# Performance work log

Measured on AMD Instinct MI355X. Metric: run time of the kernel, lower is better.

Reference implementation:

```python
import jax, jax.numpy as jnp
import numpy as np
from jax import lax

B, L, NCH, NQ, NL, FW, NCLS = 256, 3000, 4, 8, 2, 128, 5
BN_EPS = 1e-5


def setup_inputs() -> dict:
    key = jax.random.key(0)
    ks = jax.random.split(key, 24)
    rn = lambda k, shape, s=0.05: jax.random.normal(k, shape, jnp.float32) * s
    inp = {}
    inp['x'] = jax.random.normal(ks[0], (B, NCH, L), jnp.float32)
    inp['conv1_w'] = rn(ks[1], (32, NCH, 7)); inp['conv1_b'] = rn(ks[2], (32,))
    inp['bn1_g'] = 1.0 + rn(ks[3], (32,)); inp['bn1_b'] = rn(ks[3], (32,))
    inp['conv2_w'] = rn(ks[4], (64, 32, 7)); inp['conv2_b'] = rn(ks[5], (64,))
    inp['bn2_g'] = 1.0 + rn(ks[6], (64,)); inp['bn2_b'] = rn(ks[6], (64,))
    inp['conv3_w'] = rn(ks[7], (128, 64, 7)); inp['conv3_b'] = rn(ks[8], (128,))
    inp['bn3_g'] = 1.0 + rn(ks[9], (128,)); inp['bn3_b'] = rn(ks[9], (128,))
    inp['conv4_w'] = rn(ks[10], (128, 128, 7)); inp['conv4_b'] = rn(ks[11], (128,))
    inp['bn4_g'] = 1.0 + rn(ks[12], (128,)); inp['bn4_b'] = rn(ks[12], (128,))
    inp['fc_w'] = rn(ks[13], (FW, 128)); inp['fc_b'] = rn(ks[14], (FW,))
    inp['ang_w'] = rn(ks[15], (NQ, FW)); inp['ang_b'] = rn(ks[16], (NQ,))
    # TorchLayer default init: uniform in [0, 2*pi)
    inp['qw'] = jax.random.uniform(ks[17], (NL, NQ, 3), jnp.float32, 0.0, 2.0 * np.pi)
    inp['h1_w'] = rn(ks[18], (64, NQ)); inp['h1_b'] = rn(ks[19], (64,))
    inp['h2_w'] = rn(ks[20], (NCLS, 64)); inp['h2_b'] = rn(ks[21], (NCLS,))
    return inp


def _conv1d(x, w, b):
    y = lax.conv_general_dilated(x, w, (1,), [(3, 3)], dimension_numbers=('NCH', 'OIH', 'NCH'))
    return y + b[None, :, None]


def _bn(x, g, b):  # eval-mode BN: running_mean=0, running_var=1
    inv = 1.0 / np.sqrt(1.0 + BN_EPS)
    return x * (g * inv)[None, :, None] + b[None, :, None]


def _maxpool4(x):
    return lax.reduce_window(x, -jnp.inf, lax.max, (1, 1, 4), (1, 1, 4), 'VALID')


def _apply_1q(state, U, w, batched):
    # state: (B, 2**NQ); wire 0 = most significant bit (PennyLane convention)
    bs = state.shape[0]
    st = state.reshape(bs, 2 ** w, 2, -1)
    if batched:
        new = jnp.einsum('sab,slbr->slar', U, st)
    else:
        new = jnp.einsum('ab,slbr->slar', U, st)
    return new.reshape(bs, -1)


def _apply_cnot(state, c, t):
    bs = state.shape[0]
    q1, q2 = min(c, t), max(c, t)
    s = state.reshape(bs, 2 ** q1, 2, 2 ** (q2 - q1 - 1), 2, -1)
    ci, ti = (2, 4) if c < t else (4, 2)
    c0 = lax.index_in_dim(s, 0, ci, keepdims=True)
    c1 = jnp.flip(lax.index_in_dim(s, 1, ci, keepdims=True), axis=ti)
    return jnp.concatenate([c0, c1], axis=ci).reshape(bs, -1)


def _rot_matrix(phi, th, om):
    # PennyLane Rot(phi, theta, omega) = RZ(omega) RY(theta) RZ(phi)
    cm, sm = jnp.cos(th / 2), jnp.sin(th / 2)
    m00 = jnp.exp(-0.5j * (phi + om)) * cm
    m01 = -jnp.exp(0.5j * (phi - om)) * sm
    m10 = jnp.exp(-0.5j * (phi - om)) * sm
    m11 = jnp.exp(0.5j * (phi + om)) * cm
    return jnp.stack([jnp.stack([m00, m01]), jnp.stack([m10, m11])]).astype(jnp.complex64)


def _qsim(angles, qw):
    bs = angles.shape[0]
    dim = 2 ** NQ
    state = jnp.zeros((bs, dim), jnp.complex64).at[:, 0].set(1.0)
    # AngleEmbedding: RY(angle_w) on each wire (batched matrices)
    c, s = jnp.cos(angles / 2), jnp.sin(angles / 2)
    for w in range(NQ):
        U = jnp.stack([jnp.stack([c[:, w], -s[:, w]], -1),
                       jnp.stack([s[:, w], c[:, w]], -1)], -2).astype(jnp.complex64)
        state = _apply_1q(state, U, w, batched=True)
    # StronglyEntanglingLayers: Rot on each wire, then CNOT ring with range r
    for l in range(NL):
        for w in range(NQ):
            U = _rot_matrix(qw[l, w, 0], qw[l, w, 1], qw[l, w, 2])
            state = _apply_1q(state, U, w, batched=False)
        r = (l % (NQ - 1)) + 1
        for i in range(NQ):
            state = _apply_cnot(state, i, (i + r) % NQ)
    probs = state.real ** 2 + state.imag ** 2
    z = [probs.reshape(bs, 2 ** w, 2, -1)[:, :, 0].sum((1, 2))
         - probs.reshape(bs, 2 ** w, 2, -1)[:, :, 1].sum((1, 2)) for w in range(NQ)]
    return jnp.stack(z, -1)  # (B, NQ)


def reference(x, conv1_w, conv1_b, bn1_g, bn1_b, conv2_w, conv2_b, bn2_g, bn2_b,
              conv3_w, conv3_b, bn3_g, bn3_b, conv4_w, conv4_b, bn4_g, bn4_b,
              fc_w, fc_b, ang_w, ang_b, qw, h1_w, h1_b, h2_w, h2_b):
    h = jax.nn.relu(_bn(_conv1d(x, conv1_w, conv1_b), bn1_g, bn1_b))
    h = jax.nn.relu(_bn(_conv1d(h, conv2_w, conv2_b), bn2_g, bn2_b))
    h = _maxpool4(h)
    h = jax.nn.relu(_bn(_conv1d(h, conv3_w, conv3_b), bn3_g, bn3_b))
    h = _maxpool4(h)
    h = jax.nn.relu(_bn(_conv1d(h, conv4_w, conv4_b), bn4_g, bn4_b))
    h = h.mean(-1)  # AdaptiveAvgPool1d(1) + Flatten -> (B, 128)
    h = jax.nn.relu(h @ fc_w.T + fc_b)  # Dropout is identity in eval
    raw = h @ ang_w.T + ang_b
    angles = np.pi * jnp.tanh(raw)
    q = _qsim(angles, qw)
    h2 = jax.nn.relu(q @ h1_w.T + h1_b)
    return h2 @ h2_w.T + h2_b
```

## Files before the change

### kernel.cpp

```cpp
#include <hip/hip_runtime.h>
#include <hip/hip_bf16.h>

#define BN_INV 0.9999950000375f
#define PI_F   3.14159265358979f

typedef __attribute__((ext_vector_type(8))) short s16x8;
typedef __attribute__((ext_vector_type(4))) float f32x4;
typedef __attribute__((ext_vector_type(4))) unsigned short u16x4;

__device__ inline unsigned short f2bf(float f) {
  union { float f; unsigned u; } v; v.f = f;
  unsigned r = v.u + 0x7fffu + ((v.u >> 16) & 1u);
  return (unsigned short)(r >> 16);
}

__global__ __launch_bounds__(256) void k_pack(
    const float* __restrict__ w1, const float* __restrict__ w2,
    const float* __restrict__ w3, const float* __restrict__ w4,
    unsigned short* __restrict__ w1p, unsigned short* __restrict__ w2p,
    unsigned short* __restrict__ w3p, unsigned short* __restrict__ w4p,
    float* __restrict__ h4)
{
  int e = blockIdx.x * 256 + threadIdx.x;
  if (e < 2048) {
    int co = e >> 6, k = e & 63, kk = k >> 3, ci = k & 7;
    w1p[e] = (ci < 4 && kk < 7) ? f2bf(w1[co * 28 + ci * 7 + kk]) : (unsigned short)0;
  } else if (e < 16384) {
    int t = e - 2048; int co = t / 224, k = t % 224, kk = k >> 5, ci = k & 31;
    w2p[t] = f2bf(w2[co * 224 + ci * 7 + kk]);
  } else if (e < 73728) {
    int t = e - 16384; int co = t / 448, k = t % 448, kk = k >> 6, ci = k & 63;
    w3p[t] = f2bf(w3[co * 448 + ci * 7 + kk]);
  } else if (e < 188416) {
    int t = e - 73728; int co = t / 896, k = t % 896, kk = k >> 7, ci = k & 127;
    w4p[t] = f2bf(w4[co * 896 + ci * 7 + kk]);
  } else if (e < 221184) {
    h4[e - 188416] = 0.f;
  }
}

__global__ __launch_bounds__(256) void k_conv1(
    const float* __restrict__ x, const unsigned short* __restrict__ w1p,
    const float* __restrict__ cb, const float* __restrict__ bng,
    const float* __restrict__ bnb, unsigned short* __restrict__ h1t)
{
  __shared__ __align__(16) char lds[520 * 16 + 4096 + 256];
  float* scs = (float*)(lds + 520 * 16 + 4096);
  const int tid = threadIdx.x;
  const int b = blockIdx.y;
  const int l0 = blockIdx.x * 512;

  for (int r = tid; r < 519; r += 256) {
    int gr = l0 + r - 3;
    s16x8 v;
    if (gr >= 0 && gr < 3000) {
      const float* xr = x + b * 4 * 3000 + gr;
      v[0] = (short)f2bf(xr[0]);
      v[1] = (short)f2bf(xr[3000]);
      v[2] = (short)f2bf(xr[6000]);
      v[3] = (short)f2bf(xr[9000]);
      v[4] = 0; v[5] = 0; v[6] = 0; v[7] = 0;
    } else {
      for (int i = 0; i < 8; ++i) v[i] = 0;
    }
    *(s16x8*)(lds + r * 16) = v;
  }
  {
    int co = tid >> 3, c = tid & 7;
    s16x8 v = *(const s16x8*)(w1p + co * 64 + c * 8);
    *(s16x8*)(lds + 8320 + ((co * 128 + c * 16) ^ ((co & 7) << 4))) = v;
  }
  if (tid < 32) {
    float sc = bng[tid] * BN_INV;
    scs[tid * 2] = sc;
    scs[tid * 2 + 1] = fmaf(cb[tid], sc, bnb[tid]);
  }
  __syncthreads();

  const int w = tid >> 6, l = tid & 63, lr = l & 15, g = l >> 4;
  const int wp = w * 128;
  f32x4 acc[2][8];
  for (int m = 0; m < 2; ++m)
    for (int n = 0; n < 8; ++n)
      for (int i = 0; i < 4; ++i) acc[m][n][i] = 0.f;

  #pragma unroll
  for (int s = 0; s < 2; ++s) {
    s16x8 a[2], bf[8];
    #pragma unroll
    for (int m = 0; m < 2; ++m) {
      int co = m * 16 + lr;
      a[m] = *(const s16x8*)(lds + 8320 + ((co * 128 + s * 64 + g * 16) ^ ((co & 7) << 4)));
    }
    #pragma unroll
    for (int n = 0; n < 8; ++n) {
      int row = wp + n * 16 + lr + s * 4 + g;
      bf[n] = *(const s16x8*)(lds + row * 16);
    }
    #pragma unroll
    for (int m = 0; m < 2; ++m)
      #pragma unroll
      for (int n = 0; n < 8; ++n)
        acc[m][n] = __builtin_amdgcn_mfma_f32_16x16x32_bf16(a[m], bf[n], acc[m][n], 0, 0, 0);
  }

  #pragma unroll
  for (int m = 0; m < 2; ++m) {
    int co0 = m * 16 + g * 4;
    float sc[4], sh[4];
    #pragma unroll
    for (int j = 0; j < 4; ++j) { sc[j] = scs[(co0 + j) * 2]; sh[j] = scs[(co0 + j) * 2 + 1]; }
    #pragma unroll
    for (int n = 0; n < 8; ++n) {
      int gp = l0 + wp + n * 16 + lr;
      if (gp < 3000) {
        u16x4 o;
        #pragma unroll
        for (int j = 0; j < 4; ++j)
          o[j] = f2bf(fmaxf(fmaf(acc[m][n][j], sc[j], sh[j]), 0.f));
        *(u16x4*)(h1t + (b * 3000 + gp) * 32 + co0) = o;
      }
    }
  }
}

__global__ __launch_bounds__(256) void k_conv2(
    const unsigned short* __restrict__ h1t, const unsigned short* __restrict__ w2p,
    const float* __restrict__ cb, const float* __restrict__ bng,
    const float* __restrict__ bnb, unsigned short* __restrict__ h2pt)
{
  __shared__ __align__(16) char lds[46080];
  float* scs = (float*)(lds + 45568);
  const int tid = threadIdx.x, b = blockIdx.y, bg = blockIdx.x;

  for (int e = tid; e < 1792; e += 256) {
    int co = e / 28, c = e % 28;
    s16x8 v = *(const s16x8*)(w2p + co * 224 + c * 8);
    *(s16x8*)(lds + 16896 + ((co * 448 + c * 16) ^ ((co & 7) << 4))) = v;
  }
  if (tid < 64) {
    float sc = bng[tid] * BN_INV;
    scs[tid * 2] = sc;
    scs[tid * 2 + 1] = fmaf(cb[tid], sc, bnb[tid]);
  }
  {
    int l0 = bg * 1024;
    #pragma unroll
    for (int i = 0; i < 5; ++i) {
      int e = tid + i * 256;
      if (e < 1048) {
        int r = e >> 2, c = e & 3, gr = l0 - 3 + r;
        s16x8 v;
        if (gr >= 0 && gr < 3000) v = *(const s16x8*)(h1t + (b * 3000 + gr) * 32 + c * 8);
        else for (int q = 0; q < 8; ++q) v[q] = 0;
        *(s16x8*)(lds + ((r * 64 + c * 16) ^ ((r & 7) << 4))) = v;
      }
    }
  }
  __syncthreads();

  const int w = tid >> 6, l = tid & 63, lr = l & 15, g = l >> 4;
  const int wp = w * 64;

  for (int t = 0; t < 4; ++t) {
    const int l0 = bg * 1024 + t * 256;

    s16x8 xr[5];
    if (t < 3) {
      int nl0 = l0 + 256;
      #pragma unroll
      for (int i = 0; i < 5; ++i) {
        for (int q = 0; q < 8; ++q) xr[i][q] = 0;
        int e = tid + i * 256;
        if (e < 1048) {
          int r = e >> 2, c = e & 3, gr = nl0 - 3 + r;
          if (gr >= 0 && gr < 3000)
            xr[i] = *(const s16x8*)(h1t + (b * 3000 + gr) * 32 + c * 8);
        }
      }
    }

    f32x4 acc[4][4];
    for (int m = 0; m < 4; ++m)
      for (int n = 0; n < 4; ++n)
        for (int i = 0; i < 4; ++i) acc[m][n][i] = 0.f;

    #pragma unroll
    for (int s = 0; s < 7; ++s) {
      s16x8 a[4], bf[4];
      #pragma unroll
      for (int m = 0; m < 4; ++m) {
        int co = m * 16 + lr;
        a[m] = *(const s16x8*)(lds + 16896 + ((co * 448 + s * 64 + g * 16) ^ ((co & 7) << 4)));
      }
      #pragma unroll
      for (int n = 0; n < 4; ++n) {
        int row = wp + n * 16 + lr + s;
        bf[n] = *(const s16x8*)(lds + ((row * 64 + g * 16) ^ ((row & 7) << 4)));
      }
      #pragma unroll
      for (int m = 0; m < 4; ++m)
        #pragma unroll
        for (int n = 0; n < 4; ++n)
          acc[m][n] = __builtin_amdgcn_mfma_f32_16x16x32_bf16(a[m], bf[n], acc[m][n], 0, 0, 0);
    }

    #pragma unroll
    for (int m = 0; m < 4; ++m) {
      int co0 = m * 16 + g * 4;
      float sc[4], sh[4];
      #pragma unroll
      for (int j = 0; j < 4; ++j) { sc[j] = scs[(co0 + j) * 2]; sh[j] = scs[(co0 + j) * 2 + 1]; }
      #pragma unroll
      for (int n = 0; n < 4; ++n) {
        u16x4 o;
        #pragma unroll
        for (int j = 0; j < 4; ++j) {
          float tv = fmaxf(fmaf(acc[m][n][j], sc[j], sh[j]), 0.f);
          float t1 = fmaxf(tv, __shfl_xor(tv, 1));
          float t2 = fmaxf(t1, __shfl_xor(t1, 2));
          o[j] = f2bf(t2);
        }
        int pp = (l0 + wp + n * 16 + lr) >> 2;
        if ((l & 3) == 0 && pp < 750)
          *(u16x4*)(h2pt + (b * 750 + pp) * 64 + co0) = o;
      }
    }

    __syncthreads();
    if (t < 3) {
      #pragma unroll
      for (int i = 0; i < 5; ++i) {
        int e = tid + i * 256;
        if (e < 1048) {
          int r = e >> 2, c = e & 3;
          *(s16x8*)(lds + ((r * 64 + c * 16) ^ ((r & 7) << 4))) = xr[i];
        }
      }
    }
    __syncthreads();
  }
}

__global__ __launch_bounds__(256) void k_conv3(
    const unsigned short* __restrict__ h2pt, const unsigned short* __restrict__ w3p,
    const float* __restrict__ cb, const float* __restrict__ bng,
    const float* __restrict__ bnb, unsigned short* __restrict__ h3pt)
{
  __shared__ __align__(16) char lds[75776];
  float* scs = (float*)(lds + 74752);
  const int tid = threadIdx.x, b = blockIdx.y, ch = blockIdx.x;
  const int cg0 = ch * 64;

  for (int e = tid; e < 3584; e += 256) {
    int co = e / 56, c = e % 56;
    s16x8 v = *(const s16x8*)(w3p + (cg0 + co) * 448 + c * 8);
    *(s16x8*)(lds + 17408 + ((co * 896 + c * 16) ^ ((co & 7) << 4))) = v;
  }
  if (tid < 64) {
    int co = cg0 + tid;
    float sc = bng[co] * BN_INV;
    scs[tid * 2] = sc;
    scs[tid * 2 + 1] = fmaf(cb[co], sc, bnb[co]);
  }
  {
    #pragma unroll
    for (int i = 0; i < 5; ++i) {
      int e = tid + i * 256;
      if (e < 1072) {
        int r = e >> 3, c = e & 7, gr = r - 3;
        s16x8 v;
        if (gr >= 0 && gr < 750) v = *(const s16x8*)(h2pt + (b * 750 + gr) * 64 + c * 8);
        else for (int q = 0; q < 8; ++q) v[q] = 0;
        *(s16x8*)(lds + ((r * 128 + c * 16) ^ ((r & 7) << 4))) = v;
      }
    }
  }
  __syncthreads();

  const int w = tid >> 6, l = tid & 63, lr = l & 15, g = l >> 4;
  const int wp = w * 32;

  for (int t = 0; t < 6; ++t) {
    const int l0 = t * 128;

    s16x8 xr[5];
    if (t < 5) {
      int nl0 = l0 + 128;
      #pragma unroll
      for (int i = 0; i < 5; ++i) {
        for (int q = 0; q < 8; ++q) xr[i][q] = 0;
        int e = tid + i * 256;
        if (e < 1072) {
          int r = e >> 3, c = e & 7, gr = nl0 - 3 + r;
          if (gr >= 0 && gr < 750)
            xr[i] = *(const s16x8*)(h2pt + (b * 750 + gr) * 64 + c * 8);
        }
      }
    }

    f32x4 acc[4][2];
    for (int m = 0; m < 4; ++m)
      for (int n = 0; n < 2; ++n)
        for (int i = 0; i < 4; ++i) acc[m][n][i] = 0.f;

    #pragma unroll
    for (int sl = 0; sl < 14; ++sl) {
      int kk = sl >> 1, cib = (sl & 1) * 32;
      s16x8 a[4], bf[2];
      #pragma unroll
      for (int m = 0; m < 4; ++m) {
        int co = m * 16 + lr;
        a[m] = *(const s16x8*)(lds + 17408 + ((co * 896 + sl * 64 + g * 16) ^ ((co & 7) << 4)));
      }
      #pragma unroll
      for (int n = 0; n < 2; ++n) {
        int row = wp + n * 16 + lr + kk;
        bf[n] = *(const s16x8*)(lds + ((row * 128 + cib * 2 + g * 16) ^ ((row & 7) << 4)));
      }
      #pragma unroll
      for (int m = 0; m < 4; ++m)
        #pragma unroll
        for (int n = 0; n < 2; ++n)
          acc[m][n] = __builtin_amdgcn_mfma_f32_16x16x32_bf16(a[m], bf[n], acc[m][n], 0, 0, 0);
    }

    #pragma unroll
    for (int m = 0; m < 4; ++m) {
      int co0 = m * 16 + g * 4;
      float sc[4], sh[4];
      #pragma unroll
      for (int j = 0; j < 4; ++j) { sc[j] = scs[(co0 + j) * 2]; sh[j] = scs[(co0 + j) * 2 + 1]; }
      #pragma unroll
      for (int n = 0; n < 2; ++n) {
        u16x4 o;
        #pragma unroll
        for (int j = 0; j < 4; ++j) {
          float tv = fmaxf(fmaf(acc[m][n][j], sc[j], sh[j]), 0.f);
          float t1 = fmaxf(tv, __shfl_xor(tv, 1));
          float t2 = fmaxf(t1, __shfl_xor(t1, 2));
          o[j] = f2bf(t2);
        }
        int pp = (l0 + wp + n * 16 + lr) >> 2;
        if ((l & 3) == 0 && pp < 187)
          *(u16x4*)(h3pt + (b * 187 + pp) * 128 + cg0 + co0) = o;
      }
    }

    __syncthreads();
    if (t < 5) {
      #pragma unroll
      for (int i = 0; i < 5; ++i) {
        int e = tid + i * 256;
        if (e < 1072) {
          int r = e >> 3, c = e & 7;
          *(s16x8*)(lds + ((r * 128 + c * 16) ^ ((r & 7) << 4))) = xr[i];
        }
      }
    }
    __syncthreads();
  }
}

__global__ __launch_bounds__(256) void k_conv4(
    const unsigned short* __restrict__ h3pt, const unsigned short* __restrict__ w4p,
    const float* __restrict__ cb, const float* __restrict__ bng,
    const float* __restrict__ bnb, float* __restrict__ h4)
{
  __shared__ __align__(16) char lds[79872];
  float* scs = (float*)(lds + 79360);
  const int tid = threadIdx.x, b = blockIdx.y, ch = blockIdx.x;
  const int cg0 = ch * 64;

  #pragma unroll
  for (int i = 0; i < 13; ++i) {
    int e = tid + i * 256;
    if (e < 3168) {
      int r = e >> 4, c = e & 15, gr = r - 3;
      s16x8 v;
      if (gr >= 0 && gr < 187) v = *(const s16x8*)(h3pt + (b * 187 + gr) * 128 + c * 8);
      else for (int q = 0; q < 8; ++q) v[q] = 0;
      *(s16x8*)(lds + ((r * 256 + c * 16) ^ ((r & 7) << 4))) = v;
    }
  }
  for (int e = tid; e < 1792; e += 256) {
    int co = e / 28, c = e % 28;
    s16x8 v = *(const s16x8*)(w4p + (cg0 + co) * 896 + c * 8);
    *(s16x8*)(lds + 50688 + ((co * 448 + c * 16) ^ ((co & 7) << 4))) = v;
  }
  if (tid < 64) {
    int co = cg0 + tid;
    float sc = bng[co] * BN_INV;
    scs[tid * 2] = sc;
    scs[tid * 2 + 1] = fmaf(cb[co], sc, bnb[co]);
  }
  __syncthreads();

  const int w = tid >> 6, l = tid & 63, lr = l & 15, g = l >> 4;
  const int co_off = (w & 1) * 32, pos_off = (w >> 1) * 96;

  f32x4 acc[2][6];
  for (int m = 0; m < 2; ++m)
    for (int n = 0; n < 6; ++n)
      for (int i = 0; i < 4; ++i) acc[m][n][i] = 0.f;

  for (int chunk = 0; chunk < 4; ++chunk) {
    s16x8 wr[7];
    if (chunk < 3) {
      #pragma unroll
      for (int i = 0; i < 7; ++i) {
        int e = tid + i * 256;
        int co = e / 28, c = e % 28;
        wr[i] = *(const s16x8*)(w4p + (cg0 + co) * 896 + (chunk + 1) * 224 + c * 8);
      }
    }
    #pragma unroll
    for (int sl = 0; sl < 7; ++sl) {
      int k0 = chunk * 224 + sl * 32;
      int kk = k0 >> 7, cib = k0 & 127;
      s16x8 a[2], bf[6];
      #pragma unroll
      for (int m = 0; m < 2; ++m) {
        int co = co_off + m * 16 + lr;
        a[m] = *(const s16x8*)(lds + 50688 + ((co * 448 + sl * 64 + g * 16) ^ ((co & 7) << 4)));
      }
      #pragma unroll
      for (int n = 0; n < 6; ++n) {
        int row = pos_off + n * 16 + lr + kk;
        bf[n] = *(const s16x8*)(lds + ((row * 256 + cib * 2 + g * 16) ^ ((row & 7) << 4)));
      }
      #pragma unroll
      for (int m = 0; m < 2; ++m)
        #pragma unroll
        for (int n = 0; n < 6; ++n)
          acc[m][n] = __builtin_amdgcn_mfma_f32_16x16x32_bf16(a[m], bf[n], acc[m][n], 0, 0, 0);
    }
    __syncthreads();
    if (chunk < 3) {
      #pragma unroll
      for (int i = 0; i < 7; ++i) {
        int e = tid + i * 256;
        int co = e / 28, c = e % 28;
        *(s16x8*)(lds + 50688 + ((co * 448 + c * 16) ^ ((co & 7) << 4))) = wr[i];
      }
    }
    __syncthreads();
  }

  float psum[2][4];
  for (int m = 0; m < 2; ++m)
    for (int j = 0; j < 4; ++j) psum[m][j] = 0.f;
  #pragma unroll
  for (int m = 0; m < 2; ++m) {
    int col = co_off + m * 16 + g * 4;
    #pragma unroll
    for (int n = 0; n < 6; ++n) {
      int pos_g = pos_off + n * 16 + lr;
      #pragma unroll
      for (int j = 0; j < 4; ++j) {
        float tv = fmaxf(fmaf(acc[m][n][j], scs[(col + j) * 2], scs[(col + j) * 2 + 1]), 0.f);
        if (pos_g < 187) psum[m][j] += tv;
      }
    }
  }
  #pragma unroll
  for (int m = 0; m < 2; ++m)
    #pragma unroll
    for (int j = 0; j < 4; ++j) {
      float v = psum[m][j];
      v += __shfl_xor(v, 1);
      v += __shfl_xor(v, 2);
      v += __shfl_xor(v, 4);
      v += __shfl_xor(v, 8);
      if (lr == 0)
        atomicAdd(&h4[b * 128 + cg0 + co_off + m * 16 + g * 4 + j], v);
    }
}

__global__ __launch_bounds__(64) void k_head(
    const float* __restrict__ h4, const float* __restrict__ fc_w,
    const float* __restrict__ fc_b, const float* __restrict__ ang_w,
    const float* __restrict__ ang_b, const float* __restrict__ qw,
    const float* __restrict__ h1_w, const float* __restrict__ h1_b,
    const float* __restrict__ h2_w, const float* __restrict__ h2_b,
    float* __restrict__ out)
{
  const int lane = threadIdx.x;
  const int b = blockIdx.x;

  float hv0 = h4[b * 128 + lane] * (1.0f / 187.0f);
  float hv1 = h4[b * 128 + 64 + lane] * (1.0f / 187.0f);

  float a0 = fc_b[lane], a1 = fc_b[lane + 64];
  {
    const float* w0 = fc_w + lane * 128;
    const float* w1 = fc_w + (lane + 64) * 128;
    #pragma unroll
    for (int k = 0; k < 64; ++k) {
      float hk = __shfl(hv0, k);
      a0 = fmaf(hk, w0[k], a0);
      a1 = fmaf(hk, w1[k], a1);
    }
    #pragma unroll
    for (int k = 0; k < 64; ++k) {
      float hk = __shfl(hv1, k);
      a0 = fmaf(hk, w0[64 + k], a0);
      a1 = fmaf(hk, w1[64 + k], a1);
    }
  }
  float f0 = fmaxf(a0, 0.f), f1 = fmaxf(a1, 0.f);

  float rcw[8], rsw[8];
  #pragma unroll
  for (int o = 0; o < 8; ++o) {
    float p = fmaf(f0, ang_w[o * 128 + lane], f1 * ang_w[o * 128 + 64 + lane]);
    #pragma unroll
    for (int m = 1; m < 64; m <<= 1) p += __shfl_xor(p, m);
    float aa = PI_F * tanhf(ang_b[o] + p);
    rcw[o] = cosf(0.5f * aa);
    rsw[o] = sinf(0.5f * aa);
  }

  float r0, r1, r2, r3, r4, r5, r6, r7;
  {
    int gq = lane & 15;
    float phi = qw[gq * 3], th = qw[gq * 3 + 1], om = qw[gq * 3 + 2];
    float cm = cosf(0.5f * th), sm = sinf(0.5f * th);
    float ap = 0.5f * (phi + om), bm = 0.5f * (phi - om);
    float ca = cosf(ap), sa = sinf(ap), cb2 = cosf(bm), sb2 = sinf(bm);
    r0 = cm * ca;   r1 = -cm * sa;
    r2 = -sm * cb2; r3 = -sm * sb2;
    r4 = sm * cb2;  r5 = -sm * sb2;
    r6 = cm * ca;   r7 = cm * sa;
  }

  float2 st[4];
  st[0] = make_float2((lane == 0) ? 1.f : 0.f, 0.f);
  st[1] = make_float2(0.f, 0.f);
  st[2] = make_float2(0.f, 0.f);
  st[3] = make_float2(0.f, 0.f);

  auto ry_lane = [&](int lx, float c, float s) {
    #pragma unroll
    for (int j = 0; j < 4; ++j) {
      float ox = __shfl_xor(st[j].x, lx);
      float oy = __shfl_xor(st[j].y, lx);
      bool hi = (lane & lx) != 0;
      float a0x = hi ? ox : st[j].x, a0y = hi ? oy : st[j].y;
      float a1x = hi ? st[j].x : ox, a1y = hi ? st[j].y : oy;
      float cA = hi ? s : c, cB = hi ? c : -s;
      st[j].x = cA * a0x + cB * a1x;
      st[j].y = cA * a0y + cB * a1y;
    }
  };
#define RY_SLOT(J0, J1, c, s) { \
    float2 A = st[J0], B = st[J1]; \
    st[J0].x = (c) * A.x - (s) * B.x; st[J0].y = (c) * A.y - (s) * B.y; \
    st[J1].x = (s) * A.x + (c) * B.x; st[J1].y = (s) * A.y + (c) * B.y; }

  ry_lane(32, rcw[0], rsw[0]);
  ry_lane(16, rcw[1], rsw[1]);
  ry_lane(8,  rcw[2], rsw[2]);
  ry_lane(4,  rcw[3], rsw[3]);
  ry_lane(2,  rcw[4], rsw[4]);
  ry_lane(1,  rcw[5], rsw[5]);
  RY_SLOT(0, 2, rcw[6], rsw[6]); RY_SLOT(1, 3, rcw[6], rsw[6]);
  RY_SLOT(0, 1, rcw[7], rsw[7]); RY_SLOT(2, 3, rcw[7], rsw[7]);

  auto rot_lane = [&](int gi, int lx) {
    float m00x = __shfl(r0, gi), m00y = __shfl(r1, gi);
    float m01x = __shfl(r2, gi), m01y = __shfl(r3, gi);
    float m10x = __shfl(r4, gi), m10y = __shfl(r5, gi);
    float m11x = __shfl(r6, gi), m11y = __shfl(r7, gi);
    #pragma unroll
    for (int j = 0; j < 4; ++j) {
      float ox = __shfl_xor(st[j].x, lx);
      float oy = __shfl_xor(st[j].y, lx);
      bool hi = (lane & lx) != 0;
      float a0x = hi ? ox : st[j].x, a0y = hi ? oy : st[j].y;
      float a1x = hi ? st[j].x : ox, a1y = hi ? st[j].y : oy;
      float cx = hi ? m10x : m00x, cy = hi ? m10y : m00y;
      float dx = hi ? m11x : m01x, dy = hi ? m11y : m01y;
      st[j].x = cx * a0x - cy * a0y + dx * a1x - dy * a1y;
      st[j].y = cx * a0y + cy * a0x + dx * a1y + dy * a1x;
    }
  };
#define ROT_SLOT(J0, J1) { \
    float2 A = st[J0], B = st[J1]; \
    st[J0].x = m00x * A.x - m00y * A.y + m01x * B.x - m01y * B.y; \
    st[J0].y = m00x * A.y + m00y * A.x + m01x * B.y + m01y * B.x; \
    st[J1].x = m10x * A.x - m10y * A.y + m11x * B.x - m11y * B.y; \
    st[J1].y = m10x * A.y + m10y * A.x + m11x * B.y + m11y * B.x; }
  auto rot_slot = [&](int gi, int bit) {
    float m00x = __shfl(r0, gi), m00y = __shfl(r1, gi);
    float m01x = __shfl(r2, gi), m01y = __shfl(r3, gi);
    float m10x = __shfl(r4, gi), m10y = __shfl(r5, gi);
    float m11x = __shfl(r6, gi), m11y = __shfl(r7, gi);
    if (bit == 1) { ROT_SLOT(0, 2) ROT_SLOT(1, 3) }
    else          { ROT_SLOT(0, 1) ROT_SLOT(2, 3) }
  };

  auto cnot = [&](int cmask, int tmask) {
    bool cb0, cb1, cb2, cb3;
    if (cmask >= 4) {
      bool cbl = (lane & (cmask >> 2)) != 0;
      cb0 = cbl; cb1 = cbl; cb2 = cbl; cb3 = cbl;
    } else {
      cb0 = false;
      cb1 = (1 & cmask) != 0;
      cb2 = (2 & cmask) != 0;
      cb3 = (3 & cmask) != 0;
    }
    if (tmask >= 4) {
      int lx = tmask >> 2;
      { float ox = __shfl_xor(st[0].x, lx), oy = __shfl_xor(st[0].y, lx); if (cb0) { st[0].x = ox; st[0].y = oy; } }
      { float ox = __shfl_xor(st[1].x, lx), oy = __shfl_xor(st[1].y, lx); if (cb1) { st[1].x = ox; st[1].y = oy; } }
      { float ox = __shfl_xor(st[2].x, lx), oy = __shfl_xor(st[2].y, lx); if (cb2) { st[2].x = ox; st[2].y = oy; } }
      { float ox = __shfl_xor(st[3].x, lx), oy = __shfl_xor(st[3].y, lx); if (cb3) { st[3].x = ox; st[3].y = oy; } }
    } else {
      float2 o0 = st[0], o1 = st[1], o2 = st[2], o3 = st[3];
      if (tmask == 2) {
        if (cb0) st[0] = o2;
        if (cb1) st[1] = o3;
        if (cb2) st[2] = o0;
        if (cb3) st[3] = o1;
      } else {
        if (cb0) st[0] = o1;
        if (cb1) st[1] = o0;
        if (cb2) st[2] = o3;
        if (cb3) st[3] = o2;
      }
    }
  };

  #pragma unroll
  for (int lay = 0; lay < 2; ++lay) {
    rot_lane(lay * 8 + 0, 32);
    rot_lane(lay * 8 + 1, 16);
    rot_lane(lay * 8 + 2, 8);
    rot_lane(lay * 8 + 3, 4);
    rot_lane(lay * 8 + 4, 2);
    rot_lane(lay * 8 + 5, 1);
    rot_slot(lay * 8 + 6, 1);
    rot_slot(lay * 8 + 7, 0);
    int r = lay + 1;
    #pragma unroll
    for (int i = 0; i < 8; ++i) {
      int c = i, t = (i + r) & 7;
      cnot(1 << (7 - c), 1 << (7 - t));
    }
  }

  float p0 = st[0].x * st[0].x + st[0].y * st[0].y;
  float p1 = st[1].x * st[1].x + st[1].y * st[1].y;
  float p2 = st[2].x * st[2].x + st[2].y * st[2].y;
  float p3 = st[3].x * st[3].x + st[3].y * st[3].y;
  float sAll = p0 + p1 + p2 + p3;
  float zp[8];
  zp[0] = (lane & 32) ? -sAll : sAll;
  zp[1] = (lane & 16) ? -sAll : sAll;
  zp[2] = (lane & 8)  ? -sAll : sAll;
  zp[3] = (lane & 4)  ? -sAll : sAll;
  zp[4] = (lane & 2)  ? -sAll : sAll;
  zp[5] = (lane & 1)  ? -sAll : sAll;
  zp[6] = (p0 + p1) - (p2 + p3);
  zp[7] = (p0 - p1) + (p2 - p3);
  #pragma unroll
  for (int o = 0; o < 8; ++o) {
    #pragma unroll
    for (int m = 1; m < 64; m <<= 1) zp[o] += __shfl_xor(zp[o], m);
  }

  float ah = h1_b[lane];
  const float* hw = h1_w + lane * 8;
  #pragma unroll
  for (int k = 0; k < 8; ++k) ah = fmaf(zp[k], hw[k], ah);
  float hh = fmaxf(ah, 0.f);

  #pragma unroll
  for (int o = 0; o < 5; ++o) {
    float v = hh * h2_w[o * 64 + lane];
    #pragma unroll
    for (int m = 1; m < 64; m <<= 1) v += __shfl_xor(v, m);
    if (lane == 0) out[b * 5 + o] = v + h2_b[o];
  }
#undef RY_SLOT
#undef ROT_SLOT
}

extern "C" void kernel_launch(void* const* d_in, const int* in_sizes, int n_in,
                              void* d_out, int out_size, void* d_ws, size_t ws_size,
                              hipStream_t stream) {
  (void)in_sizes; (void)n_in; (void)out_size; (void)ws_size;
  const float* x    = (const float*)d_in[0];
  const float* c1w  = (const float*)d_in[1];
  const float* c1b  = (const float*)d_in[2];
  const float* b1g  = (const float*)d_in[3];
  const float* b1b  = (const float*)d_in[4];
  const float* c2w  = (const float*)d_in[5];
  const float* c2b  = (const float*)d_in[6];
  const float* b2g  = (const float*)d_in[7];
  const float* b2b  = (const float*)d_in[8];
  const float* c3w  = (const float*)d_in[9];
  const float* c3b  = (const float*)d_in[10];
  const float* b3g  = (const float*)d_in[11];
  const float* b3b  = (const float*)d_in[12];
  const float* c4w  = (const float*)d_in[13];
  const float* c4b  = (const float*)d_in[14];
  const float* b4g  = (const float*)d_in[15];
  const float* b4b  = (const float*)d_in[16];
  const float* fcw  = (const float*)d_in[17];
  const float* fcb  = (const float*)d_in[18];
  const float* angw = (const float*)d_in[19];
  const float* angb = (const float*)d_in[20];
  const float* qw   = (const float*)d_in[21];
  const float* h1w  = (const float*)d_in[22];
  const float* h1b  = (const float*)d_in[23];
  const float* h2w  = (const float*)d_in[24];
  const float* h2b  = (const float*)d_in[25];

  char* wsb = (char*)d_ws;
  unsigned short* w1p  = (unsigned short*)(wsb + 0);
  unsigned short* w2p  = (unsigned short*)(wsb + 4096);
  unsigned short* w3p  = (unsigned short*)(wsb + 32768);
  unsigned short* w4p  = (unsigned short*)(wsb + 147456);
  float*          h4   = (float*)(wsb + 393216);
  unsigned short* h1t  = (unsigned short*)(wsb + 1048576);
  unsigned short* h2pt = (unsigned short*)(wsb + 52428800);
  unsigned short* h3pt = (unsigned short*)(wsb + 79691776);

  k_pack<<<dim3(864), 256, 0, stream>>>(c1w, c2w, c3w, c4w, w1p, w2p, w3p, w4p, h4);
  k_conv1<<<dim3(6, 256), 256, 0, stream>>>(x, w1p, c1b, b1g, b1b, h1t);
  k_conv2<<<dim3(3, 256), 256, 0, stream>>>(h1t, w2p, c2b, b2g, b2b, h2pt);
  k_conv3<<<dim3(2, 256), 256, 0, stream>>>(h2pt, w3p, c3b, b3g, b3b, h3pt);
  k_conv4<<<dim3(2, 256), 256, 0, stream>>>(h3pt, w4p, c4b, b4g, b4b, h4);
  k_head<<<dim3(256), 64, 0, stream>>>(h4, fcw, fcb, angw, angb, qw,
                                       h1w, h1b, h2w, h2b, (float*)d_out);
}
```

Measured before the change: 251.9 us.

## Swap MFMA operand roles and split conv2/conv3 into one tile per block

Conv2 and conv3 now give each block a single position tile instead of looping over several tiles with register-prefetch double buffering. The grids grow from 3 and 2 blocks per batch to 12. The MFMA operands are swapped so positions map to the accumulator's row dimension. That makes the 4-wide maxpool a purely in-register max over the accumulator lanes, with no cross-lane shuffles, and conv4's mean reduction uses fewer shuffles and atomics. The cost is that weights are reloaded into LDS for every tile and stores become scalar 16-bit writes rather than 4-wide vectors.

```diff
diff --git a/kernel.cpp b/kernel.cpp
--- a/kernel.cpp
+++ b/kernel.cpp
@@ -131,8 +131,17 @@
 {
   __shared__ __align__(16) char lds[46080];
   float* scs = (float*)(lds + 45568);
-  const int tid = threadIdx.x, b = blockIdx.y, bg = blockIdx.x;
-
+  const int tid = threadIdx.x, b = blockIdx.y;
+  const int l0 = blockIdx.x * 256;
+
+  for (int e = tid; e < 1048; e += 256) {
+    int r = e >> 2, c = e & 3;
+    int gr = l0 + r - 3;
+    s16x8 v;
+    if (gr >= 0 && gr < 3000) v = *(const s16x8*)(h1t + (b * 3000 + gr) * 32 + c * 8);
+    else for (int i = 0; i < 8; ++i) v[i] = 0;
+    *(s16x8*)(lds + ((r * 64 + c * 16) ^ ((r & 7) << 4))) = v;
+  }
   for (int e = tid; e < 1792; e += 256) {
     int co = e / 28, c = e % 28;
     s16x8 v = *(const s16x8*)(w2p + co * 224 + c * 8);
@@ -143,102 +152,53 @@
     scs[tid * 2] = sc;
     scs[tid * 2 + 1] = fmaf(cb[tid], sc, bnb[tid]);
   }
-  {
-    int l0 = bg * 1024;
-    #pragma unroll
-    for (int i = 0; i < 5; ++i) {
-      int e = tid + i * 256;
-      if (e < 1048) {
-        int r = e >> 2, c = e & 3, gr = l0 - 3 + r;
-        s16x8 v;
-        if (gr >= 0 && gr < 3000) v = *(const s16x8*)(h1t + (b * 3000 + gr) * 32 + c * 8);
-        else for (int q = 0; q < 8; ++q) v[q] = 0;
-        *(s16x8*)(lds + ((r * 64 + c * 16) ^ ((r & 7) << 4))) = v;
-      }
-    }
-  }
   __syncthreads();
 
   const int w = tid >> 6, l = tid & 63, lr = l & 15, g = l >> 4;
   const int wp = w * 64;
-
-  for (int t = 0; t < 4; ++t) {
-    const int l0 = bg * 1024 + t * 256;
-
-    s16x8 xr[5];
-    if (t < 3) {
-      int nl0 = l0 + 256;
-      #pragma unroll
-      for (int i = 0; i < 5; ++i) {
-        for (int q = 0; q < 8; ++q) xr[i][q] = 0;
-        int e = tid + i * 256;
-        if (e < 1048) {
-          int r = e >> 2, c = e & 3, gr = nl0 - 3 + r;
-          if (gr >= 0 && gr < 3000)
-            xr[i] = *(const s16x8*)(h1t + (b * 3000 + gr) * 32 + c * 8);
-        }
-      }
-    }
-
-    f32x4 acc[4][4];
+  f32x4 acc[4][4];
+  for (int m = 0; m < 4; ++m)
+    for (int n = 0; n < 4; ++n)
+      for (int i = 0; i < 4; ++i) acc[m][n][i] = 0.f;
+
+  #pragma unroll
+  for (int s = 0; s < 7; ++s) {
+    s16x8 xa[4], wb[4];
+    #pragma unroll
+    for (int m = 0; m < 4; ++m) {
+      int row = wp + m * 16 + lr + s;
+      xa[m] = *(const s16x8*)(lds + ((row * 64 + g * 16) ^ ((row & 7) << 4)));
+    }
+    #pragma unroll
+    for (int n = 0; n < 4; ++n) {
+      int co = n * 16 + lr;
+      wb[n] = *(const s16x8*)(lds + 16896 + ((co * 448 + s * 64 + g * 16) ^ ((co & 7) << 4)));
+    }
+    #pragma unroll
     for (int m = 0; m < 4; ++m)
+      #pragma unroll
       for (int n = 0; n < 4; ++n)
-        for (int i = 0; i < 4; ++i) acc[m][n][i] = 0.f;
-
-    #pragma unroll
-    for (int s = 0; s < 7; ++s) {
-      s16x8 a[4], bf[4];
-      #pragma unroll
-      for (int m = 0; m < 4; ++m) {
-        int co = m * 16 + lr;
-        a[m] = *(const s16x8*)(lds + 16896 + ((co * 448 + s * 64 + g * 16) ^ ((co & 7) << 4)));
-      }
+        acc[m][n] = __builtin_amdgcn_mfma_f32_16x16x32_bf16(xa[m], wb[n], acc[m][n], 0, 0, 0);
+  }
+
+  float sc[4], sh[4];
+  #pragma unroll
+  for (int n = 0; n < 4; ++n) {
+    sc[n] = scs[(n * 16 + lr) * 2];
+    sh[n] = scs[(n * 16 + lr) * 2 + 1];
+  }
+  #pragma unroll
+  for (int m = 0; m < 4; ++m) {
+    int pp = (l0 + wp + m * 16 + g * 4) >> 2;
+    if (pp < 750) {
+      unsigned short* orow = h2pt + (b * 750 + pp) * 64 + lr;
       #pragma unroll
       for (int n = 0; n < 4; ++n) {
-        int row = wp + n * 16 + lr + s;
-        bf[n] = *(const s16x8*)(lds + ((row * 64 + g * 16) ^ ((row & 7) << 4)));
-      }
-      #pragma unroll
-      for (int m = 0; m < 4; ++m)
-        #pragma unroll
-        for (int n = 0; n < 4; ++n)
-          acc[m][n] = __builtin_amdgcn_mfma_f32_16x16x32_bf16(a[m], bf[n], acc[m][n], 0, 0, 0);
-    }
-
-    #pragma unroll
-    for (int m = 0; m < 4; ++m) {
-      int co0 = m * 16 + g * 4;
-      float sc[4], sh[4];
-      #pragma unroll
-      for (int j = 0; j < 4; ++j) { sc[j] = scs[(co0 + j) * 2]; sh[j] = scs[(co0 + j) * 2 + 1]; }
-      #pragma unroll
-      for (int n = 0; n < 4; ++n) {
-        u16x4 o;
-        #pragma unroll
-        for (int j = 0; j < 4; ++j) {
-          float tv = fmaxf(fmaf(acc[m][n][j], sc[j], sh[j]), 0.f);
-          float t1 = fmaxf(tv, __shfl_xor(tv, 1));
-          float t2 = fmaxf(t1, __shfl_xor(t1, 2));
-          o[j] = f2bf(t2);
-        }
-        int pp = (l0 + wp + n * 16 + lr) >> 2;
-        if ((l & 3) == 0 && pp < 750)
-          *(u16x4*)(h2pt + (b * 750 + pp) * 64 + co0) = o;
-      }
-    }
-
-    __syncthreads();
-    if (t < 3) {
-      #pragma unroll
-      for (int i = 0; i < 5; ++i) {
-        int e = tid + i * 256;
-        if (e < 1048) {
-          int r = e >> 2, c = e & 3;
-          *(s16x8*)(lds + ((r * 64 + c * 16) ^ ((r & 7) << 4))) = xr[i];
-        }
-      }
-    }
-    __syncthreads();
+        float v = fmaxf(fmaxf(acc[m][n][0], acc[m][n][1]),
+                        fmaxf(acc[m][n][2], acc[m][n][3]));
+        orow[n * 16] = f2bf(fmaxf(fmaf(v, sc[n], sh[n]), 0.f));
+      }
+    }
   }
 }
 
@@ -249,9 +209,18 @@
 {
   __shared__ __align__(16) char lds[75776];
   float* scs = (float*)(lds + 74752);
-  const int tid = threadIdx.x, b = blockIdx.y, ch = blockIdx.x;
-  const int cg0 = ch * 64;
-
+  const int tid = threadIdx.x, b = blockIdx.y;
+  const int tile = blockIdx.x >> 1, ch = blockIdx.x & 1;
+  const int l0 = tile * 128, cg0 = ch * 64;
+
+  for (int e = tid; e < 1072; e += 256) {
+    int r = e >> 3, c = e & 7;
+    int gr = l0 + r - 3;
+    s16x8 v;
+    if (gr >= 0 && gr < 750) v = *(const s16x8*)(h2pt + (b * 750 + gr) * 64 + c * 8);
+    else for (int i = 0; i < 8; ++i) v[i] = 0;
+    *(s16x8*)(lds + ((r * 128 + c * 16) ^ ((r & 7) << 4))) = v;
+  }
   for (int e = tid; e < 3584; e += 256) {
     int co = e / 56, c = e % 56;
     s16x8 v = *(const s16x8*)(w3p + (cg0 + co) * 448 + c * 8);
@@ -263,102 +232,54 @@
     scs[tid * 2] = sc;
     scs[tid * 2 + 1] = fmaf(cb[co], sc, bnb[co]);
   }
-  {
-    #pragma unroll
-    for (int i = 0; i < 5; ++i) {
-      int e = tid + i * 256;
-      if (e < 1072) {
-        int r = e >> 3, c = e & 7, gr = r - 3;
-        s16x8 v;
-        if (gr >= 0 && gr < 750) v = *(const s16x8*)(h2pt + (b * 750 + gr) * 64 + c * 8);
-        else for (int q = 0; q < 8; ++q) v[q] = 0;
-        *(s16x8*)(lds + ((r * 128 + c * 16) ^ ((r & 7) << 4))) = v;
-      }
-    }
-  }
   __syncthreads();
 
   const int w = tid >> 6, l = tid & 63, lr = l & 15, g = l >> 4;
   const int wp = w * 32;
-
-  for (int t = 0; t < 6; ++t) {
-    const int l0 = t * 128;
-
-    s16x8 xr[5];
-    if (t < 5) {
-      int nl0 = l0 + 128;
-      #pragma unroll
-      for (int i = 0; i < 5; ++i) {
-        for (int q = 0; q < 8; ++q) xr[i][q] = 0;
-        int e = tid + i * 256;
-        if (e < 1072) {
-          int r = e >> 3, c = e & 7, gr = nl0 - 3 + r;
-          if (gr >= 0 && gr < 750)
-            xr[i] = *(const s16x8*)(h2pt + (b * 750 + gr) * 64 + c * 8);
-        }
-      }
-    }
-
-    f32x4 acc[4][2];
-    for (int m = 0; m < 4; ++m)
-      for (int n = 0; n < 2; ++n)
-        for (int i = 0; i < 4; ++i) acc[m][n][i] = 0.f;
-
-    #pragma unroll
-    for (int sl = 0; sl < 14; ++sl) {
-      int kk = sl >> 1, cib = (sl & 1) * 32;
-      s16x8 a[4], bf[2];
-      #pragma unroll
-      for (int m = 0; m < 4; ++m) {
-        int co = m * 16 + lr;
-        a[m] = *(const s16x8*)(lds + 17408 + ((co * 896 + sl * 64 + g * 16) ^ ((co & 7) << 4)));
-      }
-      #pragma unroll
-      for (int n = 0; n < 2; ++n) {
-        int row = wp + n * 16 + lr + kk;
-        bf[n] = *(const s16x8*)(lds + ((row * 128 + cib * 2 + g * 16) ^ ((row & 7) << 4)));
-      }
-      #pragma unroll
-      for (int m = 0; m < 4; ++m)
-        #pragma unroll
-        for (int n = 0; n < 2; ++n)
-          acc[m][n] = __builtin_amdgcn_mfma_f32_16x16x32_bf16(a[m], bf[n], acc[m][n], 0, 0, 0);
-    }
-
-    #pragma unroll
-    for (int m = 0; m < 4; ++m) {
-      int co0 = m * 16 + g * 4;
-      float sc[4], sh[4];
-      #pragma unroll
-      for (int j = 0; j < 4; ++j) { sc[j] = scs[(co0 + j) * 2]; sh[j] = scs[(co0 + j) * 2 + 1]; }
-      #pragma unroll
-      for (int n = 0; n < 2; ++n) {
-        u16x4 o;
-        #pragma unroll
-        for (int j = 0; j < 4; ++j) {
-          float tv = fmaxf(fmaf(acc[m][n][j], sc[j], sh[j]), 0.f);
-          float t1 = fmaxf(tv, __shfl_xor(tv, 1));
-          float t2 = fmaxf(t1, __shfl_xor(t1, 2));
-          o[j] = f2bf(t2);
-        }
-        int pp = (l0 + wp + n * 16 + lr) >> 2;
-        if ((l & 3) == 0 && pp < 187)
-          *(u16x4*)(h3pt + (b * 187 + pp) * 128 + cg0 + co0) = o;
-      }
-    }
-
-    __syncthreads();
-    if (t < 5) {
-      #pragma unroll
-      for (int i = 0; i < 5; ++i) {
-        int e = tid + i * 256;
-        if (e < 1072) {
-          int r = e >> 3, c = e & 7;
-          *(s16x8*)(lds + ((r * 128 + c * 16) ^ ((r & 7) << 4))) = xr[i];
-        }
-      }
-    }
-    __syncthreads();
+  f32x4 acc[2][4];
+  for (int m = 0; m < 2; ++m)
+    for (int n = 0; n < 4; ++n)
+      for (int i = 0; i < 4; ++i) acc[m][n][i] = 0.f;
+
+  #pragma unroll
+  for (int sl = 0; sl < 14; ++sl) {
+    int kk = sl >> 1, cib = (sl & 1) * 32;
+    s16x8 xa[2], wb[4];
+    #pragma unroll
+    for (int m = 0; m < 2; ++m) {
+      int row = wp + m * 16 + lr + kk;
+      xa[m] = *(const s16x8*)(lds + ((row * 128 + cib * 2 + g * 16) ^ ((row & 7) << 4)));
+    }
+    #pragma unroll
+    for (int n = 0; n < 4; ++n) {
+      int co = n * 16 + lr;
+      wb[n] = *(const s16x8*)(lds + 17408 + ((co * 896 + sl * 64 + g * 16) ^ ((co & 7) << 4)));
+    }
+    #pragma unroll
+    for (int m = 0; m < 2; ++m)
+      #pragma unroll
+      for (int n = 0; n < 4; ++n)
+        acc[m][n] = __builtin_amdgcn_mfma_f32_16x16x32_bf16(xa[m], wb[n], acc[m][n], 0, 0, 0);
+  }
+
+  float sc[4], sh[4];
+  #pragma unroll
+  for (int n = 0; n < 4; ++n) {
+    sc[n] = scs[(n * 16 + lr) * 2];
+    sh[n] = scs[(n * 16 + lr) * 2 + 1];
+  }
+  #pragma unroll
+  for (int m = 0; m < 2; ++m) {
+    int pp = (l0 + wp + m * 16 + g * 4) >> 2;
+    if (pp < 187) {
+      unsigned short* orow = h3pt + (b * 187 + pp) * 128 + cg0 + lr;
+      #pragma unroll
+      for (int n = 0; n < 4; ++n) {
+        float v = fmaxf(fmaxf(acc[m][n][0], acc[m][n][1]),
+                        fmaxf(acc[m][n][2], acc[m][n][3]));
+        orow[n * 16] = f2bf(fmaxf(fmaf(v, sc[n], sh[n]), 0.f));
+      }
+    }
   }
 }
 
@@ -397,11 +318,11 @@
   __syncthreads();
 
   const int w = tid >> 6, l = tid & 63, lr = l & 15, g = l >> 4;
-  const int co_off = (w & 1) * 32, pos_off = (w >> 1) * 96;
-
-  f32x4 acc[2][6];
-  for (int m = 0; m < 2; ++m)
-    for (int n = 0; n < 6; ++n)
+  const int wp = w * 48;
+
+  f32x4 acc[3][4];
+  for (int m = 0; m < 3; ++m)
+    for (int n = 0; n < 4; ++n)
       for (int i = 0; i < 4; ++i) acc[m][n][i] = 0.f;
 
   for (int chunk = 0; chunk < 4; ++chunk) {
@@ -418,22 +339,22 @@
     for (int sl = 0; sl < 7; ++sl) {
       int k0 = chunk * 224 + sl * 32;
       int kk = k0 >> 7, cib = k0 & 127;
-      s16x8 a[2], bf[6];
-      #pragma unroll
-      for (int m = 0; m < 2; ++m) {
-        int co = co_off + m * 16 + lr;
-        a[m] = *(const s16x8*)(lds + 50688 + ((co * 448 + sl * 64 + g * 16) ^ ((co & 7) << 4)));
-      }
-      #pragma unroll
-      for (int n = 0; n < 6; ++n) {
-        int row = pos_off + n * 16 + lr + kk;
-        bf[n] = *(const s16x8*)(lds + ((row * 256 + cib * 2 + g * 16) ^ ((row & 7) << 4)));
-      }
-      #pragma unroll
-      for (int m = 0; m < 2; ++m)
+      s16x8 xa[3], wb[4];
+      #pragma unroll
+      for (int m = 0; m < 3; ++m) {
+        int row = wp + m * 16 + lr + kk;
+        xa[m] = *(const s16x8*)(lds + ((row * 256 + cib * 2 + g * 16) ^ ((row & 7) << 4)));
+      }
+      #pragma unroll
+      for (int n = 0; n < 4; ++n) {
+        int co = n * 16 + lr;
+        wb[n] = *(const s16x8*)(lds + 50688 + ((co * 448 + sl * 64 + g * 16) ^ ((co & 7) << 4)));
+      }
+      #pragma unroll
+      for (int m = 0; m < 3; ++m)
         #pragma unroll
-        for (int n = 0; n < 6; ++n)
-          acc[m][n] = __builtin_amdgcn_mfma_f32_16x16x32_bf16(a[m], bf[n], acc[m][n], 0, 0, 0);
+        for (int n = 0; n < 4; ++n)
+          acc[m][n] = __builtin_amdgcn_mfma_f32_16x16x32_bf16(xa[m], wb[n], acc[m][n], 0, 0, 0);
     }
     __syncthreads();
     if (chunk < 3) {
@@ -447,34 +368,33 @@
     __syncthreads();
   }
 
-  float psum[2][4];
-  for (int m = 0; m < 2; ++m)
-    for (int j = 0; j < 4; ++j) psum[m][j] = 0.f;
-  #pragma unroll
-  for (int m = 0; m < 2; ++m) {
-    int col = co_off + m * 16 + g * 4;
-    #pragma unroll
-    for (int n = 0; n < 6; ++n) {
-      int pos_g = pos_off + n * 16 + lr;
-      #pragma unroll
-      for (int j = 0; j < 4; ++j) {
-        float tv = fmaxf(fmaf(acc[m][n][j], scs[(col + j) * 2], scs[(col + j) * 2 + 1]), 0.f);
-        if (pos_g < 187) psum[m][j] += tv;
-      }
-    }
-  }
-  #pragma unroll
-  for (int m = 0; m < 2; ++m)
+  float sc[4], sh[4];
+  #pragma unroll
+  for (int n = 0; n < 4; ++n) {
+    sc[n] = scs[(n * 16 + lr) * 2];
+    sh[n] = scs[(n * 16 + lr) * 2 + 1];
+  }
+  float psum[4] = {0.f, 0.f, 0.f, 0.f};
+  #pragma unroll
+  for (int m = 0; m < 3; ++m) {
     #pragma unroll
     for (int j = 0; j < 4; ++j) {
-      float v = psum[m][j];
-      v += __shfl_xor(v, 1);
-      v += __shfl_xor(v, 2);
-      v += __shfl_xor(v, 4);
-      v += __shfl_xor(v, 8);
-      if (lr == 0)
-        atomicAdd(&h4[b * 128 + cg0 + co_off + m * 16 + g * 4 + j], v);
-    }
+      int pos = wp + m * 16 + g * 4 + j;
+      if (pos < 187) {
+        #pragma unroll
+        for (int n = 0; n < 4; ++n)
+          psum[n] += fmaxf(fmaf(acc[m][n][j], sc[n], sh[n]), 0.f);
+      }
+    }
+  }
+  #pragma unroll
+  for (int n = 0; n < 4; ++n) {
+    float v = psum[n];
+    v += __shfl_xor(v, 16);
+    v += __shfl_xor(v, 32);
+    if (l < 16)
+      atomicAdd(&h4[b * 128 + cg0 + n * 16 + lr], v);
+  }
 }
 
 __global__ __launch_bounds__(64) void k_head(
@@ -730,10 +650,10 @@
   unsigned short* h3pt = (unsigned short*)(wsb + 79691776);
 
   k_pack<<<dim3(864), 256, 0, stream>>>(c1w, c2w, c3w, c4w, w1p, w2p, w3p, w4p, h4);
-  k_conv1<<<dim3(6, 256), 256, 0, stream>>>(x, w1p, c1b, b1g, b1b, h1t);
-  k_conv2<<<dim3(3, 256), 256, 0, stream>>>(h1t, w2p, c2b, b2g, b2b, h2pt);
-  k_conv3<<<dim3(2, 256), 256, 0, stream>>>(h2pt, w3p, c3b, b3g, b3b, h3pt);
-  k_conv4<<<dim3(2, 256), 256, 0, stream>>>(h3pt, w4p, c4b, b4g, b4b, h4);
+  k_conv1<<<dim3(6, 256),  256, 0, stream>>>(x, w1p, c1b, b1g, b1b, h1t);
+  k_conv2<<<dim3(12, 256), 256, 0, stream>>>(h1t, w2p, c2b, b2g, b2b, h2pt);
+  k_conv3<<<dim3(12, 256), 256, 0, stream>>>(h2pt, w3p, c3b, b3g, b3b, h3pt);
+  k_conv4<<<dim3(2, 256),  256, 0, stream>>>(h3pt, w4p, c4b, b4g, b4b, h4);
   k_head<<<dim3(256), 64, 0, stream>>>(h4, fcw, fcb, angw, angb, qw,
                                        h1w, h1b, h2w, h2b, (float*)d_out);
 }
```

After: 229.6 us. 8.8% less time.
